# Kernel optimization log

Hardware: AMD Instinct MI355X
Metric: run time of the kernel (lower is better)

## Reference

```python
import jax, jax.numpy as jnp
import numpy as np
from jax import lax

K = 9          # box kernel side
PAD = K // 2   # same padding
K_SUM = float(K * K * K)


def _box_sum(x):
    """Sliding-window sum over a 9x9x9 box, zero-padded (separable 1D convs).
    x: [B, 1, D, H, W] -> same shape."""
    dn = ('NCDHW', 'OIDHW', 'NCDHW')
    for ax in range(3):  # D, H, W
        kshape = [1, 1, 1, 1, 1]
        kshape[2 + ax] = K
        w = jnp.ones(kshape, dtype=x.dtype)
        pad = [(0, 0), (0, 0), (0, 0)]
        pad[ax] = (PAD, PAD)
        x = lax.conv_general_dilated(x, w, window_strides=(1, 1, 1),
                                     padding=pad, dimension_numbers=dn)
    return x


def setup_inputs() -> dict:
    key = jax.random.key(0)
    k1, k2 = jax.random.split(key)
    shape = (2, 1, 192, 192, 192)  # [B, 1, D, H, W]
    I = jax.random.uniform(k1, shape, dtype=jnp.float32)
    J = jax.random.uniform(k2, shape, dtype=jnp.float32)
    return {"I": I, "J": J}


def reference(I, J):
    II = I * I
    JJ = J * J
    IJ = I * J
    I_sum = _box_sum(I)
    J_sum = _box_sum(J)
    II_sum = _box_sum(II)
    JJ_sum = _box_sum(JJ)
    IJ_sum = _box_sum(IJ)
    I_u = I / K_SUM
    J_u = J / K_SUM
    cross = IJ_sum - I_sum * J_u - J_sum * I_u + I_u * J_u * K_SUM
    I_var = II_sum - 2 * I_sum * I_u + I_u * I_u * K_SUM
    J_var = JJ_sum - 2 * J_sum * J_u + J_u * J_u * K_SUM
    top = cross * cross
    bottom = I_var * J_var + 1e-5
    return -jnp.mean(top / bottom)
```

## Files before the change

### kernel.cpp

```cpp
#include <hip/hip_runtime.h>
#include <hip/hip_bf16.h>

#define WDIM 192
#define PLANE (192 * 192)
#define VOL (192 * 192 * 192)
#define HC 24
#define TR (HC + 8)
#define ROWW 200
#define DC 24

__global__ void zero_out_k(float* out) { out[0] = 0.0f; }

static __device__ inline unsigned int pk_bf16(float a, float b) {
    union { __hip_bfloat162 v; unsigned int u; } cvt;
    cvt.v = __float22bfloat162_rn(make_float2(a, b));
    return cvt.u;
}
static __device__ inline float bf_lo(unsigned int u) {
    union { unsigned int u; float f; } c; c.u = u << 16; return c.f;
}
static __device__ inline float bf_hi(unsigned int u) {
    union { unsigned int u; float f; } c; c.u = u & 0xffff0000u; return c.f;
}

__global__ __launch_bounds__(192) void wh_pass(const float* __restrict__ I,
                                               const float* __restrict__ J,
                                               unsigned int* __restrict__ B) {
    __shared__ unsigned int sPK[TR * ROWW];
    const int t = threadIdx.x;
    const int d = blockIdx.x >> 3;
    const int c = blockIdx.x & 7;
    const int h0 = c * HC;

    const size_t bofs = (size_t)blockIdx.y * VOL;
    const float* Ib = I + bofs;
    const float* Jb = J + bofs;
    unsigned int* Bb = B + bofs * 3;

    const size_t dbase = (size_t)d * PLANE;

    {
        if (t < 256 - 192) {
            const int i1 = t + 192;
            const int row = i1 >> 3;
            const int p = i1 & 7;
            const int col = (p < 4) ? p : (192 + p);
            sPK[row * ROWW + col] = 0u;
        }
        const int row = t >> 3;
        const int p = t & 7;
        const int col = (p < 4) ? p : (192 + p);
        if (t < 256) sPK[row * ROWW + col] = 0u;
    }

    #pragma unroll
    for (int i = 0; i < 8; ++i) {
        const int idx4 = i * 192 + t;
        const int row  = idx4 / 48;
        const int col4 = (idx4 - row * 48) * 4;
        const int h = h0 - 4 + row;
        float4 vI = make_float4(0.f, 0.f, 0.f, 0.f);
        float4 vJ = vI;
        if (h >= 0 && h < WDIM) {
            vI = *(const float4*)(Ib + dbase + (size_t)h * WDIM + col4);
            vJ = *(const float4*)(Jb + dbase + (size_t)h * WDIM + col4);
        }
        uint4 u;
        u.x = pk_bf16(vI.x, vJ.x);
        u.y = pk_bf16(vI.y, vJ.y);
        u.z = pk_bf16(vI.z, vJ.z);
        u.w = pk_bf16(vI.w, vJ.w);
        *(uint4*)&sPK[row * ROWW + 4 + col4] = u;
    }
    __syncthreads();

    float ring0[9], ring1[9], ring2[9], ring3[9], ring4[9];
    #pragma unroll
    for (int j = 0; j < 9; ++j) { ring0[j]=0.f; ring1[j]=0.f; ring2[j]=0.f; ring3[j]=0.f; ring4[j]=0.f; }
    float s0 = 0.f, s1 = 0.f, s2 = 0.f, s3 = 0.f, s4 = 0.f;

    unsigned int uA[9], uB[9];
    #pragma unroll
    for (int k = 0; k < 9; ++k) uA[k] = sPK[0 * ROWW + t + k];

    #pragma unroll
    for (int s = 0; s < TR; ++s) {
        if (s + 1 < TR) {
            if ((s & 1) == 0) {
                #pragma unroll
                for (int k = 0; k < 9; ++k) uB[k] = sPK[(s + 1) * ROWW + t + k];
            } else {
                #pragma unroll
                for (int k = 0; k < 9; ++k) uA[k] = sPK[(s + 1) * ROWW + t + k];
            }
        }
        float w0 = 0.f, w1 = 0.f, w2 = 0.f, w3 = 0.f, w4 = 0.f;
        #pragma unroll
        for (int k = 0; k < 9; ++k) {
            const unsigned int u = ((s & 1) == 0) ? uA[k] : uB[k];
            const float a = bf_lo(u);
            const float b = bf_hi(u);
            w0 += a; w1 += b;
            w2 += a * a; w3 += b * b; w4 += a * b;
        }
        const int j = s % 9;
        s0 += w0 - ring0[j]; ring0[j] = w0;
        s1 += w1 - ring1[j]; ring1[j] = w1;
        s2 += w2 - ring2[j]; ring2[j] = w2;
        s3 += w3 - ring3[j]; ring3[j] = w3;
        s4 += w4 - ring4[j]; ring4[j] = w4;

        if (s >= 8) {
            const int h_out = h0 + s - 8;
            const size_t idx = dbase + (size_t)h_out * WDIM + t;
            uint3 q;
            q.x = pk_bf16(s0, s1);
            q.y = pk_bf16(s2, s3);
            q.z = pk_bf16(s4, 0.f);
            *(uint3*)(Bb + idx * 3) = q;
        }
    }
}

__global__ __launch_bounds__(192) void d_pass(const unsigned int* __restrict__ B,
                                              const float* __restrict__ I,
                                              const float* __restrict__ J,
                                              float* __restrict__ out) {
    const int t = threadIdx.x;
    const int h = blockIdx.x >> 3;
    const int c = blockIdx.x & 7;
    const int d0 = c * DC;
    const int base_h = h * WDIM + t;

    const size_t bofs = (size_t)blockIdx.y * VOL;
    const float* Ib = I + bofs;
    const float* Jb = J + bofs;
    const unsigned int* Bb = B + bofs * 3;

    float r0[9], r1[9], r2[9], r3[9], r4[9];
    #pragma unroll
    for (int j = 0; j < 9; ++j) { r0[j]=0.f; r1[j]=0.f; r2[j]=0.f; r3[j]=0.f; r4[j]=0.f; }
    float s0 = 0.f, s1 = 0.f, s2 = 0.f, s3 = 0.f, s4 = 0.f;

    const float inv_k = 1.0f / 729.0f;
    float local = 0.f;

    uint3 qA[8], qB[8];
    float2 cA[8], cB[8];
    #pragma unroll
    for (int i = 0; i < 8; ++i) {
        const int d_in = d0 - 4 + i;
        qA[i] = make_uint3(0u, 0u, 0u);
        if (d_in >= 0 && d_in < WDIM)
            qA[i] = *(const uint3*)(Bb + ((size_t)d_in * PLANE + base_h) * 3);
        cA[i] = make_float2(0.f, 0.f);
    }

    #pragma unroll
    for (int g = 0; g < 4; ++g) {
        if (g + 1 < 4) {
            #pragma unroll
            for (int i = 0; i < 8; ++i) {
                const int s = (g + 1) * 8 + i;
                const int d_in = d0 - 4 + s;
                uint3 v = make_uint3(0u, 0u, 0u);
                if (d_in >= 0 && d_in < WDIM)
                    v = *(const uint3*)(Bb + ((size_t)d_in * PLANE + base_h) * 3);
                const int d_out = d0 + s - 8;
                const size_t cidx = (size_t)d_out * PLANE + base_h;
                const float ci = Ib[cidx];
                const float cj = Jb[cidx];
                if ((g & 1) == 0) { qB[i] = v; cB[i] = make_float2(ci, cj); }
                else              { qA[i] = v; cA[i] = make_float2(ci, cj); }
            }
        }
        #pragma unroll
        for (int i = 0; i < 8; ++i) {
            const int s = g * 8 + i;
            const uint3 q = ((g & 1) == 0) ? qA[i] : qB[i];
            const float f0 = bf_lo(q.x), f1 = bf_hi(q.x);
            const float f2 = bf_lo(q.y), f3 = bf_hi(q.y);
            const float f4 = bf_lo(q.z);
            const int j = s % 9;
            s0 += f0 - r0[j]; r0[j] = f0;
            s1 += f1 - r1[j]; r1[j] = f1;
            s2 += f2 - r2[j]; r2[j] = f2;
            s3 += f3 - r3[j]; r3[j] = f3;
            s4 += f4 - r4[j]; r4[j] = f4;

            if (s >= 8) {
                const float2 cc = ((g & 1) == 0) ? cA[i] : cB[i];
                const float Iu = cc.x * inv_k;
                const float Ju = cc.y * inv_k;
                const float cross = s4 - s0 * Ju - s1 * Iu + Iu * Ju * 729.0f;
                const float Ivar  = s2 - 2.0f * s0 * Iu + Iu * Iu * 729.0f;
                const float Jvar  = s3 - 2.0f * s1 * Ju + Ju * Ju * 729.0f;
                local += (cross * cross) / (Ivar * Jvar + 1e-5f);
            }
        }
    }

    __shared__ float sred[192];
    sred[t] = local;
    __syncthreads();
    if (t < 64) {
        float v = sred[t] + sred[t + 64] + sred[t + 128];
        #pragma unroll
        for (int off = 32; off; off >>= 1) v += __shfl_down(v, off);
        if (t == 0) {
            atomicAdd(out, v * (-1.0f / 14155776.0f));
        }
    }
}

extern "C" void kernel_launch(void* const* d_in, const int* in_sizes, int n_in,
                              void* d_out, int out_size, void* d_ws, size_t ws_size,
                              hipStream_t stream) {
    const float* I = (const float*)d_in[0];
    const float* J = (const float*)d_in[1];
    float* out = (float*)d_out;
    unsigned int* B = (unsigned int*)d_ws;

    zero_out_k<<<1, 1, 0, stream>>>(out);

    const size_t need2 = (size_t)2 * VOL * 12;
    if (ws_size >= need2) {
        wh_pass<<<dim3(1536, 2), 192, 0, stream>>>(I, J, B);
        d_pass <<<dim3(1536, 2), 192, 0, stream>>>(B, I, J, out);
    } else {
        for (int b = 0; b < 2; ++b) {
            const float* Ib = I + (size_t)b * VOL;
            const float* Jb = J + (size_t)b * VOL;
            wh_pass<<<dim3(1536, 1), 192, 0, stream>>>(Ib, Jb, B);
            d_pass <<<dim3(1536, 1), 192, 0, stream>>>(B, Ib, Jb, out);
        }
    }
}
```

Measured before the change: 244.1 us.

## Switch packed intermediates to fp16 and use packed dot2 for W-window sums

```diff
diff --git a/kernel.cpp b/kernel.cpp
--- a/kernel.cpp
+++ b/kernel.cpp
@@ -1,32 +1,37 @@
 #include <hip/hip_runtime.h>
-#include <hip/hip_bf16.h>
 
 #define WDIM 192
 #define PLANE (192 * 192)
 #define VOL (192 * 192 * 192)
 #define HC 24
 #define TR (HC + 8)
-#define ROWW 200
+#define RWU 100
 #define DC 24
 
+typedef __fp16 h2f __attribute__((ext_vector_type(2)));
+
 __global__ void zero_out_k(float* out) { out[0] = 0.0f; }
 
-static __device__ inline unsigned int pk_bf16(float a, float b) {
-    union { __hip_bfloat162 v; unsigned int u; } cvt;
-    cvt.v = __float22bfloat162_rn(make_float2(a, b));
-    return cvt.u;
-}
-static __device__ inline float bf_lo(unsigned int u) {
-    union { unsigned int u; float f; } c; c.u = u << 16; return c.f;
-}
-static __device__ inline float bf_hi(unsigned int u) {
-    union { unsigned int u; float f; } c; c.u = u & 0xffff0000u; return c.f;
+static __device__ inline unsigned int pk_h16(float a, float b) {
+    h2f v = __builtin_amdgcn_cvt_pkrtz(a, b);
+    return __builtin_bit_cast(unsigned int, v);
+}
+static __device__ inline float h_lo(unsigned int u) {
+    h2f v = __builtin_bit_cast(h2f, u); return (float)v.x;
+}
+static __device__ inline float h_hi(unsigned int u) {
+    h2f v = __builtin_bit_cast(h2f, u); return (float)v.y;
+}
+static __device__ inline float dot2u(unsigned int a, unsigned int b, float c) {
+    return __builtin_amdgcn_fdot2(__builtin_bit_cast(h2f, a),
+                                  __builtin_bit_cast(h2f, b), c, false);
 }
 
 __global__ __launch_bounds__(192) void wh_pass(const float* __restrict__ I,
                                                const float* __restrict__ J,
                                                unsigned int* __restrict__ B) {
-    __shared__ unsigned int sPK[TR * ROWW];
+    __shared__ unsigned int sI[TR * RWU];
+    __shared__ unsigned int sJ[TR * RWU];
     const int t = threadIdx.x;
     const int d = blockIdx.x >> 3;
     const int c = blockIdx.x & 7;
@@ -39,18 +44,13 @@
 
     const size_t dbase = (size_t)d * PLANE;
 
-    {
-        if (t < 256 - 192) {
-            const int i1 = t + 192;
-            const int row = i1 >> 3;
-            const int p = i1 & 7;
-            const int col = (p < 4) ? p : (192 + p);
-            sPK[row * ROWW + col] = 0u;
-        }
-        const int row = t >> 3;
-        const int p = t & 7;
-        const int col = (p < 4) ? p : (192 + p);
-        if (t < 256) sPK[row * ROWW + col] = 0u;
+    for (int n = t; n < 256; n += 192) {
+        const int row = n >> 3;
+        const int p = n & 7;
+        unsigned int* dst = (p < 4) ? sI : sJ;
+        const int q = p & 3;
+        const int col = (q < 2) ? q : (96 + q);
+        dst[row * RWU + col] = 0u;
     }
 
     #pragma unroll
@@ -65,44 +65,78 @@
             vI = *(const float4*)(Ib + dbase + (size_t)h * WDIM + col4);
             vJ = *(const float4*)(Jb + dbase + (size_t)h * WDIM + col4);
         }
-        uint4 u;
-        u.x = pk_bf16(vI.x, vJ.x);
-        u.y = pk_bf16(vI.y, vJ.y);
-        u.z = pk_bf16(vI.z, vJ.z);
-        u.w = pk_bf16(vI.w, vJ.w);
-        *(uint4*)&sPK[row * ROWW + 4 + col4] = u;
+        uint2 uI, uJ;
+        uI.x = pk_h16(vI.x, vI.y); uI.y = pk_h16(vI.z, vI.w);
+        uJ.x = pk_h16(vJ.x, vJ.y); uJ.y = pk_h16(vJ.z, vJ.w);
+        const int ui = row * RWU + 2 + (col4 >> 1);
+        *(uint2*)&sI[ui] = uI;
+        *(uint2*)&sJ[ui] = uJ;
     }
     __syncthreads();
+
+    const int tb = t >> 1;
+    const int odd = t & 1;
+    const unsigned int ONESF = 0x3C003C00u;
+    const unsigned int ones0 = odd ? 0x3C000000u : ONESF;
+    const unsigned int ones4 = odd ? ONESF : 0x00003C00u;
+    const unsigned int keep0 = odd ? 0xFFFF0000u : 0xFFFFFFFFu;
+    const unsigned int keep4 = odd ? 0xFFFFFFFFu : 0x0000FFFFu;
 
     float ring0[9], ring1[9], ring2[9], ring3[9], ring4[9];
     #pragma unroll
     for (int j = 0; j < 9; ++j) { ring0[j]=0.f; ring1[j]=0.f; ring2[j]=0.f; ring3[j]=0.f; ring4[j]=0.f; }
     float s0 = 0.f, s1 = 0.f, s2 = 0.f, s3 = 0.f, s4 = 0.f;
 
-    unsigned int uA[9], uB[9];
-    #pragma unroll
-    for (int k = 0; k < 9; ++k) uA[k] = sPK[0 * ROWW + t + k];
+    unsigned int AI[5], AJ[5], BI[5], BJ[5];
+    #pragma unroll
+    for (int p = 0; p < 5; ++p) { AI[p] = sI[tb + p]; AJ[p] = sJ[tb + p]; }
 
     #pragma unroll
     for (int s = 0; s < TR; ++s) {
         if (s + 1 < TR) {
+            const int base = (s + 1) * RWU + tb;
             if ((s & 1) == 0) {
                 #pragma unroll
-                for (int k = 0; k < 9; ++k) uB[k] = sPK[(s + 1) * ROWW + t + k];
+                for (int p = 0; p < 5; ++p) { BI[p] = sI[base + p]; BJ[p] = sJ[base + p]; }
             } else {
                 #pragma unroll
-                for (int k = 0; k < 9; ++k) uA[k] = sPK[(s + 1) * ROWW + t + k];
+                for (int p = 0; p < 5; ++p) { AI[p] = sI[base + p]; AJ[p] = sJ[base + p]; }
             }
         }
-        float w0 = 0.f, w1 = 0.f, w2 = 0.f, w3 = 0.f, w4 = 0.f;
-        #pragma unroll
-        for (int k = 0; k < 9; ++k) {
-            const unsigned int u = ((s & 1) == 0) ? uA[k] : uB[k];
-            const float a = bf_lo(u);
-            const float b = bf_hi(u);
-            w0 += a; w1 += b;
-            w2 += a * a; w3 += b * b; w4 += a * b;
-        }
+        const unsigned int c0 = ((s & 1) == 0) ? AI[0] : BI[0];
+        const unsigned int c1 = ((s & 1) == 0) ? AI[1] : BI[1];
+        const unsigned int c2 = ((s & 1) == 0) ? AI[2] : BI[2];
+        const unsigned int c3 = ((s & 1) == 0) ? AI[3] : BI[3];
+        const unsigned int c4 = ((s & 1) == 0) ? AI[4] : BI[4];
+        const unsigned int e0 = ((s & 1) == 0) ? AJ[0] : BJ[0];
+        const unsigned int e1 = ((s & 1) == 0) ? AJ[1] : BJ[1];
+        const unsigned int e2 = ((s & 1) == 0) ? AJ[2] : BJ[2];
+        const unsigned int e3 = ((s & 1) == 0) ? AJ[3] : BJ[3];
+        const unsigned int e4 = ((s & 1) == 0) ? AJ[4] : BJ[4];
+
+        const unsigned int mI0 = c0 & keep0, mI4 = c4 & keep4;
+        const unsigned int mJ0 = e0 & keep0, mJ4 = e4 & keep4;
+
+        float w0 = dot2u(c0, ones0, 0.f);
+        w0 = dot2u(c1, ONESF, w0); w0 = dot2u(c2, ONESF, w0);
+        w0 = dot2u(c3, ONESF, w0); w0 = dot2u(c4, ones4, w0);
+
+        float w1 = dot2u(e0, ones0, 0.f);
+        w1 = dot2u(e1, ONESF, w1); w1 = dot2u(e2, ONESF, w1);
+        w1 = dot2u(e3, ONESF, w1); w1 = dot2u(e4, ones4, w1);
+
+        float w2 = dot2u(mI0, c0, 0.f);
+        w2 = dot2u(c1, c1, w2); w2 = dot2u(c2, c2, w2);
+        w2 = dot2u(c3, c3, w2); w2 = dot2u(mI4, c4, w2);
+
+        float w3 = dot2u(mJ0, e0, 0.f);
+        w3 = dot2u(e1, e1, w3); w3 = dot2u(e2, e2, w3);
+        w3 = dot2u(e3, e3, w3); w3 = dot2u(mJ4, e4, w3);
+
+        float w4 = dot2u(mI0, e0, 0.f);
+        w4 = dot2u(c1, e1, w4); w4 = dot2u(c2, e2, w4);
+        w4 = dot2u(c3, e3, w4); w4 = dot2u(mI4, e4, w4);
+
         const int j = s % 9;
         s0 += w0 - ring0[j]; ring0[j] = w0;
         s1 += w1 - ring1[j]; ring1[j] = w1;
@@ -114,9 +148,9 @@
             const int h_out = h0 + s - 8;
             const size_t idx = dbase + (size_t)h_out * WDIM + t;
             uint3 q;
-            q.x = pk_bf16(s0, s1);
-            q.y = pk_bf16(s2, s3);
-            q.z = pk_bf16(s4, 0.f);
+            q.x = pk_h16(s0, s1);
+            q.y = pk_h16(s2, s3);
+            q.z = pk_h16(s4, 0.f);
             *(uint3*)(Bb + idx * 3) = q;
         }
     }
@@ -178,9 +212,9 @@
         for (int i = 0; i < 8; ++i) {
             const int s = g * 8 + i;
             const uint3 q = ((g & 1) == 0) ? qA[i] : qB[i];
-            const float f0 = bf_lo(q.x), f1 = bf_hi(q.x);
-            const float f2 = bf_lo(q.y), f3 = bf_hi(q.y);
-            const float f4 = bf_lo(q.z);
+            const float f0 = h_lo(q.x), f1 = h_hi(q.x);
+            const float f2 = h_lo(q.y), f3 = h_hi(q.y);
+            const float f4 = h_lo(q.z);
             const int j = s % 9;
             s0 += f0 - r0[j]; r0[j] = f0;
             s1 += f1 - r1[j]; r1[j] = f1;
```

New measurement: 231.6 us. 5.1% less time.
